# Performance work log

Hardware: AMD Instinct MI355X
Metric: run time of the kernel (lower is better)

## Reference

```python
import jax, jax.numpy as jnp
import numpy as np

N = 4_194_304  # total observations
NBAND = 8      # photometric bands


def setup_inputs() -> dict:
    key = jax.random.key(0)
    ks = jax.random.split(key, 6)
    t = jnp.sort(jax.random.uniform(ks[0], (N,), dtype=jnp.float32) * 10000.0)
    band = jax.random.randint(ks[1], (N,), 0, NBAND)
    y = jax.random.normal(ks[2], (N,), dtype=jnp.float32) * 0.5
    diag = jax.random.uniform(ks[3], (N,), dtype=jnp.float32) * 0.1 + 0.01
    log_amp_delta = jax.random.normal(ks[4], (NBAND - 1,), dtype=jnp.float32) * 0.1
    lag = jax.random.uniform(ks[5], (NBAND - 1,), dtype=jnp.float32) * 5.0
    # exponential (DRW) celerite term: k(tau) = a * exp(-c * tau)
    log_kernel_param = jnp.array([0.0, -3.0], dtype=jnp.float32)
    return {"t": t, "band": band, "y": y, "diag": diag,
            "log_amp_delta": log_amp_delta, "lag": lag,
            "log_kernel_param": log_kernel_param}


def reference(t, band, y, diag, log_amp_delta, lag, log_kernel_param):
    # amp/lag transforms: prepend 0 for the reference band (jnp.insert at 0)
    log_amps = jnp.concatenate([jnp.zeros((1,), log_amp_delta.dtype), log_amp_delta])
    lags = jnp.concatenate([jnp.zeros((1,), lag.dtype), lag])

    # lag-shift times per band, then sort (GP requires sorted inputs)
    new_t = t - lags[band]
    inds = jnp.argsort(new_t)
    ts, bs, ys, ds = new_t[inds], band[inds], y[inds], diag[inds]

    # multiband kernel: K_ij = amp_i * amp_j * a * exp(-c * |t_i - t_j|) + diag_i * delta_ij
    amps = jnp.exp(log_amps)[bs]                 # [N]
    a = jnp.exp(log_kernel_param[0])
    c = jnp.exp(log_kernel_param[1])
    A = ds + a * amps * amps                     # diagonal of K
    U = a * amps                                 # low-rank left factor
    V = amps                                     # low-rank right factor
    dt = jnp.diff(ts, prepend=ts[:1])            # dt[0] = 0
    phi = jnp.exp(-c * dt)                       # transfer factor between neighbors

    # celerite O(N) Cholesky + forward solve (single real term -> scalar state)
    def step(carry, xs):
        Sp, fp = carry                           # Sp = S_{n-1} + D W^2, fp = f_{n-1} + W z
        A_n, U_n, V_n, phi_n, r_n = xs
        S = phi_n * phi_n * Sp
        D = A_n - U_n * U_n * S
        W = (V_n - U_n * S) / D
        f = phi_n * fp
        z = r_n - U_n * f
        return (S + D * W * W, f + W * z), (D, z)

    init = (jnp.zeros((), ys.dtype), jnp.zeros((), ys.dtype))
    _, (D, z) = jax.lax.scan(step, init, (A, U, V, phi, ys))

    n = ys.shape[0]
    log2pi = jnp.log(2 * jnp.pi).astype(ys.dtype)
    logp = -0.5 * (jnp.sum(z * z / D) + jnp.sum(jnp.log(D)) + n * log2pi)
    return -logp  # LCModel.__call__ returns negative log-probability
```

## Files before the change

### kernel.cpp

```cpp
#include <hip/hip_runtime.h>
#include <hip/hip_bf16.h>
#include <hip/hip_fp16.h>
#include <math.h>

#define NBAND 8
#define K1_THREADS 1024
#define CHUNK 128
#define HALO  128
#define TILE  16
#define OUTBLK 1024
#define MCAP   1280
#define SEG    32
#define NSEG   128
#define NPART  512

struct Params {
  float lags[NBAND];
  float inv_amp[NBAND];
  float inv_amp2[NBAND];
  float a, c, kphi1, kphi2;
  int bandstart[NBAND];
  int nb[NBAND];
};

__device__ __forceinline__ unsigned f2u(float f) {
  unsigned b = __float_as_uint(f);
  return b ^ ((b >> 31) ? 0xFFFFFFFFu : 0x80000000u);
}
__device__ __forceinline__ float u2f(unsigned u) {
  unsigned m = (u & 0x80000000u) ? 0x80000000u : 0xFFFFFFFFu;
  return __uint_as_float(u ^ m);
}

__global__ void k1_hist(const int* __restrict__ band, int* __restrict__ cnt,
                        int* __restrict__ segsum) {
  __shared__ int wc[16][NBAND];
  int tid = threadIdx.x;
  int i = blockIdx.x * K1_THREADS + tid;
  int b = band[i];
  int lane = tid & 63, w = tid >> 6;
#pragma unroll
  for (int bb = 0; bb < NBAND; ++bb) {
    unsigned long long m = __ballot(b == bb);
    if (lane == bb) wc[w][bb] = __popcll(m);
  }
  __syncthreads();
  if (tid < NBAND) {
    int s = 0;
#pragma unroll
    for (int w2 = 0; w2 < 16; ++w2) s += wc[w2][tid];
    cnt[blockIdx.x * NBAND + tid] = s;
    atomicAdd(&segsum[(blockIdx.x >> 5) * NBAND + tid], s);
  }
}

__global__ void k2b_scan(const int* __restrict__ segsum, int* __restrict__ segbase,
                         Params* __restrict__ P,
                         const float* __restrict__ lad, const float* __restrict__ lag,
                         const float* __restrict__ lkp) {
  __shared__ int sd[NSEG * NBAND];
  __shared__ int tot[NBAND], bstart[NBAND];
  int tid = threadIdx.x;
  if (tid == 0) {
    P->lags[0] = 0.f;
    P->inv_amp[0] = 1.f;
    P->inv_amp2[0] = 1.f;
    for (int j = 0; j < NBAND - 1; ++j) {
      P->lags[j + 1] = lag[j];
      float ia = expf(-lad[j]);
      P->inv_amp[j + 1] = ia;
      P->inv_amp2[j + 1] = ia * ia;
    }
    float a = expf(lkp[0]);
    float c = expf(lkp[1]);
    P->a = a;
    P->c = c;
    P->kphi1 = -c * 1.4426950408889634f;
    P->kphi2 = -2.f * c * 1.4426950408889634f;
  }
  int b = tid & 7, seg = tid >> 3;
  int sum = segsum[tid];
  int val = sum;
  sd[tid] = val;
  __syncthreads();
  for (int off = 1; off < NSEG; off <<= 1) {
    int yv = (seg >= off) ? sd[tid - off * NBAND] : 0;
    __syncthreads();
    val += yv;
    sd[tid] = val;
    __syncthreads();
  }
  if (seg == NSEG - 1) tot[b] = val;
  __syncthreads();
  if (tid == 0) {
    int g = 0;
    for (int bb = 0; bb < NBAND; ++bb) {
      bstart[bb] = g;
      P->bandstart[bb] = g;
      P->nb[bb] = tot[bb];
      g += tot[bb];
    }
  }
  __syncthreads();
  segbase[tid] = bstart[b] + (val - sum);
}

__global__ void k2c_boff(const int* __restrict__ cnt, const int* __restrict__ segbase,
                         int* __restrict__ boff) {
  int s = blockIdx.x * 256 + threadIdx.x;
  if (s >= NSEG * NBAND) return;
  int b = s & 7, seg = s >> 3;
  int base = seg * SEG;
  int run = segbase[s];
  for (int u = 0; u < SEG; ++u) {
    int idx = (base + u) * NBAND + b;
    int x = cnt[idx];
    boff[idx] = run;
    run += x;
  }
}

__global__ void k3_scatter(const float* __restrict__ t, const int* __restrict__ band,
                           const float* __restrict__ y, const float* __restrict__ dg,
                           const int* __restrict__ boff, const Params* __restrict__ P,
                           unsigned long long* __restrict__ rec8) {
  __shared__ int wc[16][NBAND];
  __shared__ int sboff[NBAND];
  int tid = threadIdx.x;
  int bid = blockIdx.x;
  int i = bid * K1_THREADS + tid;
  int b = band[i];
  float v = t[i] - P->lags[b];
  int lane = tid & 63, w = tid >> 6;
  int lower = 0;
#pragma unroll
  for (int bb = 0; bb < NBAND; ++bb) {
    unsigned long long m = __ballot(b == bb);
    if (lane == bb) wc[w][bb] = __popcll(m);
    if (b == bb) lower = __popcll(m & ((1ull << lane) - 1ull));
  }
  if (tid < NBAND) sboff[tid] = boff[bid * NBAND + tid];
  __syncthreads();
  int base2 = 0;
  for (int w2 = 0; w2 < w; ++w2) base2 += wc[w2][b];
  int pos = sboff[b] + base2 + lower;
  float yp = y[i] * P->inv_amp[b];
  float dp = dg[i] * P->inv_amp2[b];
  unsigned yx = __float_as_uint(yp);
  unsigned yb = (yx + 0x7FFFu + ((yx >> 16) & 1u)) >> 16;
  unsigned db = (unsigned)__half_as_ushort(__float2half(dp));
  unsigned pay = (yb << 16) | db;
  rec8[pos] = ((unsigned long long)f2u(v) << 32) | pay;
}

__global__ __launch_bounds__(256) void k4_merge(const unsigned long long* __restrict__ rec8,
                                                const Params* __restrict__ P,
                                                float2* __restrict__ out8, int nout) {
  __shared__ unsigned long long bufA[MCAP];
  __shared__ unsigned long long bufB[MCAP];
  __shared__ int cut2[2][NBAND];
  __shared__ int klo[NBAND], offs[NBAND + 1];
  __shared__ int sbs[NBAND];
  __shared__ long R0s;
  int tid = threadIdx.x;
  int o = blockIdx.x;
  if (tid < NBAND) sbs[tid] = P->bandstart[tid];
  if (tid < 16) {
    int b = tid & 7, which = tid >> 3;
    int oo = o + which;
    int res;
    if (oo == 0) res = 0;
    else if (oo >= nout) res = P->nb[b];
    else {
      float vmin = u2f((unsigned)(rec8[P->bandstart[0]] >> 32));
      float vmax = u2f((unsigned)(rec8[P->bandstart[0] + P->nb[0] - 1] >> 32));
#pragma unroll
      for (int bb = 1; bb < NBAND; ++bb) {
        vmin = fminf(vmin, u2f((unsigned)(rec8[P->bandstart[bb]] >> 32)));
        vmax = fmaxf(vmax, u2f((unsigned)(rec8[P->bandstart[bb] + P->nb[bb] - 1] >> 32)));
      }
      float v = vmin + (float)((double)(vmax - vmin) * oo / nout);
      unsigned svu = f2u(v);
      const unsigned long long* p = rec8 + P->bandstart[b];
      int lo = 0, hi = P->nb[b];
      while (lo < hi) {
        int mid = (lo + hi) >> 1;
        if ((unsigned)(p[mid] >> 32) < svu) lo = mid + 1; else hi = mid;
      }
      res = lo;
    }
    cut2[which][b] = res;
  }
  __syncthreads();
  if (tid == 0) {
    int s = 0;
    long r0 = 0;
    for (int b = 0; b < NBAND; ++b) {
      klo[b] = cut2[0][b];
      offs[b] = s;
      s += cut2[1][b] - cut2[0][b];
      r0 += cut2[0][b];
    }
    offs[NBAND] = s;
    R0s = r0;
  }
  __syncthreads();
  int M = offs[NBAND];
  if (M > MCAP) return;
  int ro[NBAND + 1];
#pragma unroll
  for (int b = 0; b <= NBAND; ++b) ro[b] = offs[b];
  for (int p = tid; p < M; p += 256) {
    int b = 0;
#pragma unroll
    for (int bb = 1; bb < NBAND; ++bb) b += (p >= ro[bb]);
    int w = p - ro[b];
    bufA[p] = rec8[sbs[b] + klo[b] + w];
  }
  __syncthreads();
#pragma unroll
  for (int r = 0; r < 3; ++r) {
    const unsigned long long* src = (r == 1) ? bufB : bufA;
    unsigned long long* dst = (r == 1) ? bufA : bufB;
    int h = 1 << r;
    int tpm = 64 << r;
    int mi = tid / tpm, tt = tid % tpm;
    int g = mi * 2 * h;
    int a1 = offs[g], a2 = offs[g + h], a3 = offs[g + 2 * h];
    int n1 = a2 - a1, n2 = a3 - a2;
    int total = n1 + n2;
    int e0 = (int)((long)tt * total / tpm);
    int e1 = (int)((long)(tt + 1) * total / tpm);
    int lo = max(0, e0 - n2), hi = min(e0, n1);
    while (lo < hi) {
      int mid = (lo + hi) >> 1;
      if (src[a1 + mid] < src[a2 + (e0 - mid) - 1]) lo = mid + 1; else hi = mid;
    }
    int i = lo, j = e0 - lo;
    unsigned long long x = (i < n1) ? src[a1 + i] : ~0ull;
    unsigned long long yv = (j < n2) ? src[a2 + j] : ~0ull;
    for (int k = e0; k < e1; ++k) {
      bool tk = x < yv;
      dst[a1 + k] = tk ? x : yv;
      if (tk) { ++i; x = (i < n1) ? src[a1 + i] : ~0ull; }
      else    { ++j; yv = (j < n2) ? src[a2 + j] : ~0ull; }
    }
    __syncthreads();
  }
  long R0 = R0s;
  for (int p = tid; p < M; p += 256) {
    unsigned long long rec = bufB[p];
    out8[R0 + p] = make_float2(u2f((unsigned)(rec >> 32)),
                               __uint_as_float((unsigned)rec));
  }
}

struct ScanState {
  float Sp, fp, tprev, s1, s2;
};

template <bool ACCUM>
__device__ __forceinline__ void step_one(float2 v, ScanState& st, float a, float a2,
                                         float k1c, float k2c) {
  float t = v.x;
  unsigned pv = __float_as_uint(v.y);
  float yv = __uint_as_float(pv & 0xFFFF0000u);
  float d = __half2float(__ushort_as_half((unsigned short)(pv & 0xFFFFu)));
  float dt = t - st.tprev;
  st.tprev = t;
  float e2 = __builtin_amdgcn_exp2f(k2c * dt);
  float e1 = __builtin_amdgcn_exp2f(k1c * dt);
  float Aa = d + a;
  float c1 = d - a;
  float x = e2 * st.Sp;
  float D = fmaf(-a2, x, Aa);
  float r = __builtin_amdgcn_rcpf(D);
  float num = fmaf(c1, x, 1.0f);
  st.Sp = num * r;
  float f = e1 * st.fp;
  float z = fmaf(-a, f, yv);
  float Wn = fmaf(-a, x, 1.0f);
  float W = Wn * r;
  st.fp = fmaf(W, z, f);
  if (ACCUM) {
    st.s1 = fmaf(z * z, r, st.s1);
    st.s2 += __builtin_amdgcn_logf(D);
  }
}

template <bool ACCUM>
__device__ __forceinline__ void run_range(const float2* __restrict__ q, long s, long e,
                                          ScanState& st, float a, float a2, float k1c,
                                          float k2c) {
  float2 A[TILE], B[TILE];
#pragma unroll
  for (int u = 0; u < TILE; ++u) A[u] = q[s + u];
  for (long tb = s; tb < e; tb += 2 * TILE) {
#pragma unroll
    for (int u = 0; u < TILE; ++u) B[u] = q[tb + TILE + u];
#pragma unroll
    for (int u = 0; u < TILE; ++u) step_one<ACCUM>(A[u], st, a, a2, k1c, k2c);
#pragma unroll
    for (int u = 0; u < TILE; ++u) A[u] = q[tb + 2 * TILE + u];
#pragma unroll
    for (int u = 0; u < TILE; ++u) step_one<ACCUM>(B[u], st, a, a2, k1c, k2c);
  }
}

__global__ __launch_bounds__(64, 1) void k5_scan(const float2* __restrict__ q,
                                                 const Params* __restrict__ P,
                                                 double2* __restrict__ part) {
  int k = blockIdx.x * 64 + threadIdx.x;
  long base = (long)k * CHUNK;
  float a = P->a, a2 = a * a, k1c = P->kphi1, k2c = P->kphi2;
  ScanState st;
  st.Sp = 0.f;
  st.fp = 0.f;
  st.s1 = 0.f;
  st.s2 = 0.f;
  long s0 = (k == 0) ? base : (base - HALO);
  st.tprev = q[s0].x;
  if (k > 0) run_range<false>(q, base - HALO, base, st, a, a2, k1c, k2c);
  run_range<true>(q, base, base + CHUNK, st, a, a2, k1c, k2c);
  float s1 = st.s1, s2 = st.s2;
#pragma unroll
  for (int off = 32; off > 0; off >>= 1) {
    s1 += __shfl_down(s1, off);
    s2 += __shfl_down(s2, off);
  }
  if (threadIdx.x == 0) part[blockIdx.x] = make_double2((double)s1, (double)s2);
}

__global__ void k6_final(const double2* __restrict__ part, const Params* __restrict__ P,
                         const float* __restrict__ lad, float* __restrict__ out, long n) {
  int tid = threadIdx.x;
  double s1 = 0.0, s2 = 0.0;
  for (int u = tid; u < NPART; u += 64) {
    double2 p = part[u];
    s1 += p.x;
    s2 += p.y;
  }
#pragma unroll
  for (int off = 32; off > 0; off >>= 1) {
    s1 += __shfl_down(s1, off);
    s2 += __shfl_down(s2, off);
  }
  if (tid == 0) {
    double ampc = 0.0;
    for (int b = 1; b < NBAND; ++b) ampc += (double)P->nb[b] * (double)lad[b - 1];
    double r = 0.5 * (s1 + s2 * 0.6931471805599453 + (double)n * 1.8378770664093453)
               + ampc;
    out[0] = (float)r;
  }
}

extern "C" void kernel_launch(void* const* d_in, const int* in_sizes, int n_in,
                              void* d_out, int out_size, void* d_ws, size_t ws_size,
                              hipStream_t stream) {
  const float* t = (const float*)d_in[0];
  const int* band = (const int*)d_in[1];
  const float* y = (const float*)d_in[2];
  const float* dg = (const float*)d_in[3];
  const float* lad = (const float*)d_in[4];
  const float* lag = (const float*)d_in[5];
  const float* lkp = (const float*)d_in[6];
  float* out = (float*)d_out;
  long N = in_sizes[0];

  char* ws = (char*)d_ws;
  Params* P = (Params*)(ws + 0);
  double2* part = (double2*)(ws + 4096);
  int* segsum = (int*)(ws + 16384);
  int* segbase = (int*)(ws + 20480);
  int* cnt = (int*)(ws + 24576);
  int* boff = (int*)(ws + 155648);
  long nblk = N / K1_THREADS;
  int nout = (int)(N / OUTBLK);
  float2* out8 = (float2*)(ws + 524288);
  unsigned long long* rec8 = (unsigned long long*)(ws + 524288 + (size_t)N * 8);

  hipMemsetAsync(segsum, 0, 4096, stream);
  k1_hist<<<(int)nblk, K1_THREADS, 0, stream>>>(band, cnt, segsum);
  k2b_scan<<<1, NSEG * NBAND, 0, stream>>>(segsum, segbase, P, lad, lag, lkp);
  k2c_boff<<<(NSEG * NBAND + 255) / 256, 256, 0, stream>>>(cnt, segbase, boff);
  k3_scatter<<<(int)nblk, K1_THREADS, 0, stream>>>(t, band, y, dg, boff, P, rec8);
  k4_merge<<<nout, 256, 0, stream>>>(rec8, P, out8, nout);
  long T = N / CHUNK;
  k5_scan<<<(int)(T / 64), 64, 0, stream>>>(out8, P, part);
  k6_final<<<1, 64, 0, stream>>>(part, P, lad, out, N);
}
```

Before: 203.7 us.

## Double merge block size and use bitonic 16-element merge per thread

Doubles the output block per merge kernel (OUTBLK 2048, larger shared buffers) and replaces the serial branchy per-thread merge loop with a merge-path split at fixed 16-element offsets, then a branch-free bitonic merge network on 32-bit keys. The goal is to cut divergent serial merging and per-block overhead. The tradeoffs are more shared memory per block and lower occupancy. With 256 threads and 16 elements each, coverage depends on the larger block sizes matching. Comparing only the high 32 bits may also change how equal keys are ordered.

New measurement: 214.4 us. 1.05x slower.

```diff
diff --git a/kernel.cpp b/kernel.cpp
--- a/kernel.cpp
+++ b/kernel.cpp
@@ -8,8 +8,8 @@
 #define CHUNK 128
 #define HALO  128
 #define TILE  16
-#define OUTBLK 1024
-#define MCAP   1280
+#define OUTBLK 2048
+#define MCAP   2432
 #define SEG    32
 #define NSEG   128
 #define NPART  512
@@ -30,6 +30,9 @@
 __device__ __forceinline__ float u2f(unsigned u) {
   unsigned m = (u & 0x80000000u) ? 0x80000000u : 0xFFFFFFFFu;
   return __uint_as_float(u ^ m);
+}
+__device__ __forceinline__ unsigned hi32(unsigned long long r) {
+  return (unsigned)(r >> 32);
 }
 
 __global__ void k1_hist(const int* __restrict__ band, int* __restrict__ cnt,
@@ -172,12 +175,12 @@
     if (oo == 0) res = 0;
     else if (oo >= nout) res = P->nb[b];
     else {
-      float vmin = u2f((unsigned)(rec8[P->bandstart[0]] >> 32));
-      float vmax = u2f((unsigned)(rec8[P->bandstart[0] + P->nb[0] - 1] >> 32));
+      float vmin = u2f(hi32(rec8[P->bandstart[0]]));
+      float vmax = u2f(hi32(rec8[P->bandstart[0] + P->nb[0] - 1]));
 #pragma unroll
       for (int bb = 1; bb < NBAND; ++bb) {
-        vmin = fminf(vmin, u2f((unsigned)(rec8[P->bandstart[bb]] >> 32)));
-        vmax = fmaxf(vmax, u2f((unsigned)(rec8[P->bandstart[bb] + P->nb[bb] - 1] >> 32)));
+        vmin = fminf(vmin, u2f(hi32(rec8[P->bandstart[bb]])));
+        vmax = fmaxf(vmax, u2f(hi32(rec8[P->bandstart[bb] + P->nb[bb] - 1])));
       }
       float v = vmin + (float)((double)(vmax - vmin) * oo / nout);
       unsigned svu = f2u(v);
@@ -185,7 +188,7 @@
       int lo = 0, hi = P->nb[b];
       while (lo < hi) {
         int mid = (lo + hi) >> 1;
-        if ((unsigned)(p[mid] >> 32) < svu) lo = mid + 1; else hi = mid;
+        if (hi32(p[mid]) < svu) lo = mid + 1; else hi = mid;
       }
       res = lo;
     }
@@ -229,29 +232,46 @@
     int a1 = offs[g], a2 = offs[g + h], a3 = offs[g + 2 * h];
     int n1 = a2 - a1, n2 = a3 - a2;
     int total = n1 + n2;
-    int e0 = (int)((long)tt * total / tpm);
-    int e1 = (int)((long)(tt + 1) * total / tpm);
-    int lo = max(0, e0 - n2), hi = min(e0, n1);
-    while (lo < hi) {
-      int mid = (lo + hi) >> 1;
-      if (src[a1 + mid] < src[a2 + (e0 - mid) - 1]) lo = mid + 1; else hi = mid;
-    }
-    int i = lo, j = e0 - lo;
-    unsigned long long x = (i < n1) ? src[a1 + i] : ~0ull;
-    unsigned long long yv = (j < n2) ? src[a2 + j] : ~0ull;
-    for (int k = e0; k < e1; ++k) {
-      bool tk = x < yv;
-      dst[a1 + k] = tk ? x : yv;
-      if (tk) { ++i; x = (i < n1) ? src[a1 + i] : ~0ull; }
-      else    { ++j; yv = (j < n2) ? src[a2 + j] : ~0ull; }
+    int e0 = tt * 16;
+    if (e0 < total) {
+      int lo = max(0, e0 - n2), hi = min(e0, n1);
+      while (lo < hi) {
+        int mid = (lo + hi) >> 1;
+        if (hi32(src[a1 + mid]) < hi32(src[a2 + (e0 - mid) - 1])) lo = mid + 1;
+        else hi = mid;
+      }
+      int i = lo, j = e0 - lo;
+      unsigned long long L[16];
+#pragma unroll
+      for (int k = 0; k < 16; ++k) {
+        unsigned long long av = (i + k < n1) ? src[a1 + i + k] : ~0ull;
+        int jb = j + 15 - k;
+        unsigned long long bv = (jb < n2) ? src[a2 + jb] : ~0ull;
+        L[k] = (hi32(av) < hi32(bv)) ? av : bv;
+      }
+#pragma unroll
+      for (int d = 8; d > 0; d >>= 1) {
+#pragma unroll
+        for (int k = 0; k < 16; ++k) {
+          if ((k & d) == 0) {
+            unsigned long long x = L[k], z = L[k + d];
+            bool sw = hi32(z) < hi32(x);
+            L[k] = sw ? z : x;
+            L[k + d] = sw ? x : z;
+          }
+        }
+      }
+      int cnt16 = min(16, total - e0);
+#pragma unroll
+      for (int k = 0; k < 16; ++k)
+        if (k < cnt16) dst[a1 + e0 + k] = L[k];
     }
     __syncthreads();
   }
   long R0 = R0s;
   for (int p = tid; p < M; p += 256) {
     unsigned long long rec = bufB[p];
-    out8[R0 + p] = make_float2(u2f((unsigned)(rec >> 32)),
-                               __uint_as_float((unsigned)rec));
+    out8[R0 + p] = make_float2(u2f(hi32(rec)), __uint_as_float((unsigned)rec));
   }
 }
 
```
